# Kernel optimization log

Measured on AMD Instinct MI355X. Metric: run time of the kernel, lower is better.

Reference implementation:

```python
import jax, jax.numpy as jnp
import numpy as np

EPS = 1e-5
P, B, T, C = 2, 8, 1024, 1024
H = 4 * C

def layernorm(x, g, b):
    mu = jnp.mean(x, axis=-1, keepdims=True)
    var = jnp.var(x, axis=-1, keepdims=True)
    return (x - mu) * jax.lax.rsqrt(var + EPS) * g + b

def time_shift(x):
    # ZeroPad2d((0,0,1,-1)): xx[t] = x[t-1], xx[0] = 0 along the T axis
    pad = [(0, 0)] * (x.ndim - 2) + [(1, 0), (0, 0)]
    return jnp.pad(x, pad)[..., :-1, :]

def wkv(time_decay, time_first, k, v):
    # Faithful port of the RWKV-v4 CUDA WKV scan (numerically stable form).
    # k, v: [N, T, C]; time_decay/time_first: [C]
    w = -jnp.exp(time_decay)  # decay (negative)
    u = time_first
    kT = jnp.moveaxis(k, 1, 0)  # [T, N, C]
    vT = jnp.moveaxis(v, 1, 0)
    N = k.shape[0]
    Cc = k.shape[2]

    def step(carry, kv):
        aa, bb, pp = carry
        kk, vv = kv
        ww = u + kk
        p = jnp.maximum(pp, ww)
        e1 = jnp.exp(pp - p)
        e2 = jnp.exp(ww - p)
        y = (e1 * aa + e2 * vv) / (e1 * bb + e2)
        ww2 = w + pp
        p2 = jnp.maximum(ww2, kk)
        e1b = jnp.exp(ww2 - p2)
        e2b = jnp.exp(kk - p2)
        return (e1b * aa + e2b * vv, e1b * bb + e2b, p2), y

    init = (jnp.zeros((N, Cc), jnp.float32), jnp.zeros((N, Cc), jnp.float32),
            jnp.full((N, Cc), -1e38, jnp.float32))
    _, yT = jax.lax.scan(step, init, (kT, vT))
    return jnp.moveaxis(yT, 0, 1)  # [N, T, C]


def setup_inputs() -> dict:
    key = jax.random.key(0)
    ks = jax.random.split(key, 20)
    f32 = jnp.float32
    layer_id, n_layer = 1, 12
    ratio_0_to_1 = layer_id / (n_layer - 1)
    ratio_1_to_almost0 = 1.0 - layer_id / n_layer
    xcurve = (np.arange(C, dtype=np.float32) / C).reshape(1, 1, C)
    decay_speed = -5 + 8 * (np.arange(C, dtype=np.float32) / (C - 1)) ** (0.7 + 1.3 * ratio_0_to_1)
    zigzag = (np.array([(i + 1) % 3 - 1 for i in range(C)], dtype=np.float32)) * 0.5
    time_first = np.ones(C, dtype=np.float32) * np.log(0.3) + zigzag
    mk = np.stack([xcurve ** ratio_1_to_almost0 for _ in range(P)], 0)  # [P,1,1,C]
    mv = np.stack([xcurve ** ratio_1_to_almost0 + 0.3 * ratio_0_to_1 for _ in range(P)], 0)
    mr = np.stack([xcurve ** (0.5 * ratio_1_to_almost0) for _ in range(P)], 0)
    s = 0.02
    return {
        'x': jax.random.normal(ks[0], (P, B, T, C), f32),
        'ln1_g': jnp.ones((C,), f32), 'ln1_b': jnp.zeros((C,), f32),
        'ln2_g': jnp.ones((C,), f32), 'ln2_b': jnp.zeros((C,), f32),
        'time_decay': jnp.asarray(decay_speed, f32),
        'time_first': jnp.asarray(time_first, f32),
        'att_mix_k': jnp.asarray(mk, f32), 'att_mix_v': jnp.asarray(mv, f32),
        'att_mix_r': jnp.asarray(mr, f32),
        'Wk': jax.random.normal(ks[1], (C, C), f32) * s,
        'Wv': jax.random.normal(ks[2], (C, C), f32) * s,
        'Wr': jax.random.normal(ks[3], (C, C), f32) * s,
        'Wo': jax.random.normal(ks[4], (C, C), f32) * s,
        'cm_mix_k': jnp.asarray(mk, f32), 'cm_mix_r': jnp.asarray(mk, f32),
        'Wck': jax.random.normal(ks[5], (H, C), f32) * s,
        'Wcr': jax.random.normal(ks[6], (C, C), f32) * s,
        'Wcv': jax.random.normal(ks[7], (C, H), f32) * s,
    }


def reference(x, ln1_g, ln1_b, ln2_g, ln2_b, time_decay, time_first,
              att_mix_k, att_mix_v, att_mix_r, Wk, Wv, Wr, Wo,
              cm_mix_k, cm_mix_r, Wck, Wcr, Wcv):
    p, b, t, c = x.shape
    # --- TimeMix branch: x = x + Wo @ (sigmoid(r) * WKV(k, v)) ---
    h = layernorm(x, ln1_g, ln1_b)
    xx = time_shift(h)
    xk = h * att_mix_k + xx * (1 - att_mix_k)
    xv = h * att_mix_v + xx * (1 - att_mix_v)
    xr = h * att_mix_r + xx * (1 - att_mix_r)
    k = jnp.einsum('pbtc,dc->pbtd', xk, Wk)
    v = jnp.einsum('pbtc,dc->pbtd', xv, Wv)
    sr = jax.nn.sigmoid(jnp.einsum('pbtc,dc->pbtd', xr, Wr))
    y = wkv(time_decay, time_first,
            k.reshape(p * b, t, c), v.reshape(p * b, t, c)).reshape(p, b, t, c)
    x = x + jnp.einsum('pbtc,dc->pbtd', sr * y, Wo)
    # --- ChannelMix branch ---
    h = layernorm(x, ln2_g, ln2_b)
    xx = time_shift(h)
    xk = h * cm_mix_k + xx * (1 - cm_mix_k)
    xr = h * cm_mix_r + xx * (1 - cm_mix_r)
    kk = jnp.einsum('pbtc,hc->pbth', xk, Wck)
    kk = jnp.square(jax.nn.relu(kk))
    kv = jnp.einsum('pbth,ch->pbtc', kk, Wcv)
    out = jax.nn.sigmoid(jnp.einsum('pbtc,dc->pbtd', xr, Wcr)) * kv
    return x + out
```

## Files before the change

kernel.cpp:

```cpp
#include <hip/hip_runtime.h>

#define T_SEQ 1024
#define C_DIM 1024
#define H_DIM 4096
#define M_ROWS 16384
#define CHUNKS 16
#define CLEN 64

typedef _Float16 f16x8 __attribute__((ext_vector_type(8)));
typedef _Float16 f16x4 __attribute__((ext_vector_type(4)));
typedef float    f32x4 __attribute__((ext_vector_type(4)));

#define AS1 __attribute__((address_space(1)))
#define AS3 __attribute__((address_space(3)))

__device__ __forceinline__ void gload_lds16(const void* g, void* l) {
  __builtin_amdgcn_global_load_lds((const AS1 void*)g, (AS3 void*)l, 16, 0, 0);
}

__device__ __forceinline__ float sigmoidf_(float x) {
  return 1.0f / (1.0f + __expf(-x));
}

__global__ __launch_bounds__(256) void cvt_kernel(const float* __restrict__ in,
                                                  _Float16* __restrict__ out, int n4) {
  int i = blockIdx.x * 256 + threadIdx.x;
  if (i >= n4) return;
  f32x4 v = reinterpret_cast<const f32x4*>(in)[i];
  f16x4 o;
  o[0] = (_Float16)v[0]; o[1] = (_Float16)v[1];
  o[2] = (_Float16)v[2]; o[3] = (_Float16)v[3];
  reinterpret_cast<f16x4*>(out)[i] = o;
}

__global__ __launch_bounds__(256) void ln_kernel(const float* __restrict__ x,
    const float* __restrict__ g, const float* __restrict__ b,
    _Float16* __restrict__ h) {
  const int row  = blockIdx.x * 4 + (threadIdx.x >> 6);
  const int lane = threadIdx.x & 63;
  const f32x4* xr = reinterpret_cast<const f32x4*>(x + (size_t)row * C_DIM);
  f32x4 v[4];
  float s = 0.f, sq = 0.f;
#pragma unroll
  for (int i = 0; i < 4; ++i) {
    v[i] = xr[i * 64 + lane];
#pragma unroll
    for (int j = 0; j < 4; ++j) { s += v[i][j]; sq += v[i][j] * v[i][j]; }
  }
#pragma unroll
  for (int off = 32; off > 0; off >>= 1) {
    s  += __shfl_xor(s, off, 64);
    sq += __shfl_xor(sq, off, 64);
  }
  const float mu   = s * (1.0f / C_DIM);
  const float var  = sq * (1.0f / C_DIM) - mu * mu;
  const float rstd = rsqrtf(var + 1e-5f);
  const f32x4* g4 = reinterpret_cast<const f32x4*>(g);
  const f32x4* b4 = reinterpret_cast<const f32x4*>(b);
  f16x4* h4 = reinterpret_cast<f16x4*>(h + (size_t)row * C_DIM);
#pragma unroll
  for (int i = 0; i < 4; ++i) {
    f32x4 gg = g4[i * 64 + lane];
    f32x4 bb = b4[i * 64 + lane];
    f16x4 o;
#pragma unroll
    for (int j = 0; j < 4; ++j)
      o[j] = (_Float16)((v[i][j] - mu) * rstd * gg[j] + bb[j]);
    h4[i * 64 + lane] = o;
  }
}

__global__ __launch_bounds__(256) void mix3_kernel(const _Float16* __restrict__ h,
    const float* __restrict__ mk, const float* __restrict__ mv, const float* __restrict__ mr,
    _Float16* __restrict__ xk, _Float16* __restrict__ xv, _Float16* __restrict__ xr) {
  const int i  = blockIdx.x * 256 + threadIdx.x;
  const int m  = i >> 7;
  const int c0 = (i & 127) << 3;
  const int p  = m >> 13;
  const int t  = m & (T_SEQ - 1);
  const f16x8* h8 = reinterpret_cast<const f16x8*>(h);
  f16x8 hc = h8[i];
  f16x8 hp;
#pragma unroll
  for (int j = 0; j < 8; ++j) hp[j] = (_Float16)0.f;
  if (t) hp = h8[i - 128];
  f16x8 ok, ov, orr;
#pragma unroll
  for (int j = 0; j < 8; ++j) {
    const float hcf = (float)hc[j], hpf = (float)hp[j];
    const float a = mk[p * C_DIM + c0 + j];
    const float c = mv[p * C_DIM + c0 + j];
    const float d = mr[p * C_DIM + c0 + j];
    ok[j]  = (_Float16)(hcf * a + hpf * (1.f - a));
    ov[j]  = (_Float16)(hcf * c + hpf * (1.f - c));
    orr[j] = (_Float16)(hcf * d + hpf * (1.f - d));
  }
  reinterpret_cast<f16x8*>(xk)[i] = ok;
  reinterpret_cast<f16x8*>(xv)[i] = ov;
  reinterpret_cast<f16x8*>(xr)[i] = orr;
}

__global__ __launch_bounds__(256) void mix2_kernel(const _Float16* __restrict__ h,
    const float* __restrict__ mk, const float* __restrict__ mr,
    _Float16* __restrict__ xk, _Float16* __restrict__ xr) {
  const int i  = blockIdx.x * 256 + threadIdx.x;
  const int m  = i >> 7;
  const int c0 = (i & 127) << 3;
  const int p  = m >> 13;
  const int t  = m & (T_SEQ - 1);
  const f16x8* h8 = reinterpret_cast<const f16x8*>(h);
  f16x8 hc = h8[i];
  f16x8 hp;
#pragma unroll
  for (int j = 0; j < 8; ++j) hp[j] = (_Float16)0.f;
  if (t) hp = h8[i - 128];
  f16x8 ok, orr;
#pragma unroll
  for (int j = 0; j < 8; ++j) {
    const float hcf = (float)hc[j], hpf = (float)hp[j];
    const float a = mk[p * C_DIM + c0 + j];
    const float d = mr[p * C_DIM + c0 + j];
    ok[j]  = (_Float16)(hcf * a + hpf * (1.f - a));
    orr[j] = (_Float16)(hcf * d + hpf * (1.f - d));
  }
  reinterpret_cast<f16x8*>(xk)[i] = ok;
  reinterpret_cast<f16x8*>(xr)[i] = orr;
}

__global__ __launch_bounds__(1024, 1) void wkv_kernel(const _Float16* __restrict__ k,
    const _Float16* __restrict__ v, const _Float16* __restrict__ r,
    const float* __restrict__ td, const float* __restrict__ tf,
    _Float16* __restrict__ a_out) {
  __shared__ float sA[CHUNKS][64];
  __shared__ float sB[CHUNKS][64];
  __shared__ float sP[CHUNKS][64];
  const int tid   = threadIdx.x;
  const int chunk = tid >> 6;
  const int ch    = tid & 63;
  const int n     = blockIdx.x >> 4;
  const int cg    = blockIdx.x & 15;
  const int c     = cg * 64 + ch;
  const float w = -__expf(td[c]);
  const float u = tf[c];
  const size_t cbase = (size_t)n * T_SEQ * C_DIM + (size_t)chunk * CLEN * C_DIM + c;

  float aa = 0.f, bb = 0.f, pp = -1e38f;
  for (int s = 0; s < CLEN; ++s) {
    const size_t idx = cbase + (size_t)s * C_DIM;
    const float kk = (float)k[idx];
    const float vv = (float)v[idx];
    const float ww2 = w + pp;
    const float p2  = fmaxf(ww2, kk);
    const float e1b = __expf(ww2 - p2);
    const float e2b = __expf(kk - p2);
    aa = e1b * aa + e2b * vv;
    bb = e1b * bb + e2b;
    pp = p2;
  }
  sA[chunk][ch] = aa; sB[chunk][ch] = bb; sP[chunk][ch] = pp;
  __syncthreads();

  if (chunk == 0) {
    float pa = 0.f, pb = 0.f, ppr = -1e38f;
    const float wL = w * (float)CLEN;
    for (int j = 0; j < CHUNKS; ++j) {
      const float la = sA[j][ch], lb = sB[j][ch], lp = sP[j][ch];
      sA[j][ch] = pa; sB[j][ch] = pb; sP[j][ch] = ppr;
      const float dp = wL + ppr;
      const float np = fmaxf(dp, lp);
      const float e1 = __expf(dp - np);
      const float e2 = __expf(lp - np);
      pa  = e1 * pa + e2 * la;
      pb  = e1 * pb + e2 * lb;
      ppr = np;
    }
  }
  __syncthreads();

  aa = sA[chunk][ch]; bb = sB[chunk][ch]; pp = sP[chunk][ch];
  for (int s = 0; s < CLEN; ++s) {
    const size_t idx = cbase + (size_t)s * C_DIM;
    const float kk = (float)k[idx];
    const float vv = (float)v[idx];
    const float ww = u + kk;
    const float p  = fmaxf(pp, ww);
    const float e1 = __expf(pp - p);
    const float e2 = __expf(ww - p);
    const float yv = __fdividef(e1 * aa + e2 * vv, e1 * bb + e2);
    const float sr = sigmoidf_((float)r[idx]);
    a_out[idx] = (_Float16)(sr * yv);
    const float ww2 = w + pp;
    const float p2  = fmaxf(ww2, kk);
    const float e1b = __expf(ww2 - p2);
    const float e2b = __expf(kk - p2);
    aa = e1b * aa + e2b * vv;
    bb = e1b * bb + e2b;
    pp = p2;
  }
}

#define GBAR() do { __builtin_amdgcn_sched_barrier(0); \
                    __builtin_amdgcn_s_barrier(); \
                    __builtin_amdgcn_sched_barrier(0); } while (0)
#define WVN(n) do { asm volatile("s_waitcnt vmcnt(" #n ")" ::: "memory"); \
                    __builtin_amdgcn_sched_barrier(0); } while (0)
#define WL0()  do { asm volatile("s_waitcnt lgkmcnt(0)" ::: "memory"); \
                    __builtin_amdgcn_sched_barrier(0); } while (0)
#define STAGE(op, SRC, row0, k0, bb) do { \
    _Pragma("unroll") \
    for (int c_ = 0; c_ < 2; ++c_) { \
      gload_lds16((SRC) + (size_t)((row0) + c_ * 64) * K + (k0), \
                  &lds[bb][op][((size_t)((row0) + c_ * 64) << 6) + dbase]); \
    } } while (0)
#define RD_A(mh) do { \
    _Pragma("unroll") for (int i_ = 0; i_ < 4; ++i_) \
    _Pragma("unroll") for (int k_ = 0; k_ < 2; ++k_) \
      af[i_][k_] = *reinterpret_cast<const f16x8*>( \
        &lds[b][0][((wr * 128 + (mh) * 64 + i_ * 16 + frow) << 6) + \
                   (((k_ << 5) + fk) ^ fxorh)]); \
  } while (0)
#define RD_B(nh) do { \
    _Pragma("unroll") for (int j_ = 0; j_ < 2; ++j_) \
    _Pragma("unroll") for (int k_ = 0; k_ < 2; ++k_) \
      bf[j_][k_] = *reinterpret_cast<const f16x8*>( \
        &lds[b][1][((wcn * 64 + (nh) * 32 + j_ * 16 + frow) << 6) + \
                   (((k_ << 5) + fk) ^ fxorh)]); \
  } while (0)
#define MM(mh, nh) do { \
    __builtin_amdgcn_s_setprio(1); \
    _Pragma("unroll") for (int k_ = 0; k_ < 2; ++k_) \
    _Pragma("unroll") for (int i_ = 0; i_ < 4; ++i_) \
    _Pragma("unroll") for (int j_ = 0; j_ < 2; ++j_) \
      acc[(mh) * 4 + i_][(nh) * 2 + j_] = __builtin_amdgcn_mfma_f32_16x16x32_f16( \
        af[i_][k_], bf[j_][k_], acc[(mh) * 4 + i_][(nh) * 2 + j_], 0, 0, 0); \
    __builtin_amdgcn_s_setprio(0); \
  } while (0)

template<int EPI>
__global__ __launch_bounds__(512, 2) void gemm_nt_256(
    const _Float16* __restrict__ A, const _Float16* __restrict__ B,
    void* __restrict__ Cv, const float* __restrict__ X,
    const _Float16* __restrict__ KV, int M, int N, int K) {
  __shared__ _Float16 lds[2][2][256 * 64];
  const int tid  = threadIdx.x;
  const int wave = tid >> 6;
  const int lane = tid & 63;
  const int wr   = wave >> 2;
  const int wcn  = wave & 3;

  const unsigned nwx  = gridDim.x;
  const unsigned pery = gridDim.y >> 3;
  const unsigned id   = blockIdx.y * nwx + blockIdx.x;
  const unsigned xcd  = id & 7;
  const unsigned loc  = id >> 3;
  const size_t m0 = (size_t)(xcd * pery + loc / nwx) * 256;
  const size_t n0 = (size_t)(loc % nwx) * 256;

  const int srow  = tid >> 3;
  const int scolh = ((tid & 7) ^ (srow & 7)) << 3;
  const size_t dbase = (size_t)(srow & ~7) << 6;
  const _Float16* sA = A + (m0 + srow) * (size_t)K + scolh;
  const _Float16* sB = B + (n0 + srow) * (size_t)K + scolh;

  const int frow  = lane & 15;
  const int fk    = (lane >> 4) << 3;
  const int fxorh = (frow & 7) << 3;

  f32x4 acc[8][4];
#pragma unroll
  for (int i = 0; i < 8; ++i)
#pragma unroll
    for (int j = 0; j < 4; ++j) acc[i][j] = (f32x4){0.f, 0.f, 0.f, 0.f};

  STAGE(0, sA, 0, 0, 0); STAGE(0, sA, 128, 0, 0);
  STAGE(1, sB, 0, 0, 0); STAGE(1, sB, 128, 0, 0);

  const int NT = K >> 6;
  for (int t = 0; t < NT; ++t) {
    const int b  = t & 1;
    const int nb = b ^ 1;
    const int k1 = (t + 1) << 6;
    if (t + 1 < NT) {
      STAGE(0, sA, 0, k1, nb); STAGE(0, sA, 128, k1, nb);
      STAGE(1, sB, 0, k1, nb); STAGE(1, sB, 128, k1, nb);
      WVN(8);
    } else {
      WVN(0);
    }
    GBAR();
    f16x8 af[4][2], bf[2][2];
    RD_A(0); RD_B(0); WL0(); MM(0, 0);
    RD_B(1);          WL0(); MM(0, 1);
    RD_A(1); RD_B(0); WL0(); MM(1, 0);
    RD_B(1);          WL0(); MM(1, 1);
    GBAR();
  }

  const int ecol  = lane & 15;
  const int erow4 = (lane >> 4) * 4;
#pragma unroll
  for (int mf = 0; mf < 8; ++mf)
#pragma unroll
    for (int nf = 0; nf < 4; ++nf) {
      const size_t rbase = m0 + (size_t)(wr * 128 + mf * 16 + erow4);
      const size_t cc    = n0 + (size_t)(wcn * 64 + nf * 16 + ecol);
#pragma unroll
      for (int r = 0; r < 4; ++r) {
        const float val = acc[mf][nf][r];
        const size_t off = (rbase + r) * (size_t)N + cc;
        if constexpr (EPI == 0) {
          ((_Float16*)Cv)[off] = (_Float16)val;
        } else if constexpr (EPI == 1) {
          const float tq = fmaxf(val, 0.f);
          ((_Float16*)Cv)[off] = (_Float16)(tq * tq);
        } else if constexpr (EPI == 2) {
          ((float*)Cv)[off] = val + X[off];
        } else {
          ((float*)Cv)[off] = X[off] + sigmoidf_(val) * (float)KV[off];
        }
      }
    }
}

extern "C" void kernel_launch(void* const* d_in, const int* in_sizes, int n_in,
                              void* d_out, int out_size, void* d_ws, size_t ws_size,
                              hipStream_t stream) {
  const float* x      = (const float*)d_in[0];
  const float* ln1_g  = (const float*)d_in[1];
  const float* ln1_b  = (const float*)d_in[2];
  const float* ln2_g  = (const float*)d_in[3];
  const float* ln2_b  = (const float*)d_in[4];
  const float* tdec   = (const float*)d_in[5];
  const float* tfirst = (const float*)d_in[6];
  const float* amk    = (const float*)d_in[7];
  const float* amv    = (const float*)d_in[8];
  const float* amr    = (const float*)d_in[9];
  const float* Wk     = (const float*)d_in[10];
  const float* Wv     = (const float*)d_in[11];
  const float* Wr     = (const float*)d_in[12];
  const float* Wo     = (const float*)d_in[13];
  const float* cmk    = (const float*)d_in[14];
  const float* cmr    = (const float*)d_in[15];
  const float* Wck    = (const float*)d_in[16];
  const float* Wcr    = (const float*)d_in[17];
  const float* Wcv    = (const float*)d_in[18];

  char* ws = (char*)d_ws;
  const size_t SZ = (size_t)M_ROWS * C_DIM * sizeof(_Float16);
  _Float16* B0 = (_Float16*)(ws + 0 * SZ);
  _Float16* B1 = (_Float16*)(ws + 1 * SZ);
  _Float16* B2 = (_Float16*)(ws + 2 * SZ);
  _Float16* B3 = (_Float16*)(ws + 3 * SZ);
  _Float16* B4 = (_Float16*)(ws + 4 * SZ);
  _Float16* B5 = (_Float16*)(ws + 5 * SZ);
  _Float16* B6 = (_Float16*)(ws + 6 * SZ);
  _Float16* wWk  = (_Float16*)(ws + 7 * SZ);
  _Float16* wWv  = wWk  + (size_t)C_DIM * C_DIM;
  _Float16* wWr  = wWv  + (size_t)C_DIM * C_DIM;
  _Float16* wWo  = wWr  + (size_t)C_DIM * C_DIM;
  _Float16* wWcr = wWo  + (size_t)C_DIM * C_DIM;
  _Float16* wWck = wWcr + (size_t)C_DIM * C_DIM;
  _Float16* wWcv = wWck + (size_t)H_DIM * C_DIM;

  auto cvt = [&](const float* src, _Float16* dst, size_t n) {
    const int n4 = (int)(n / 4);
    cvt_kernel<<<dim3((n4 + 255) / 256), dim3(256), 0, stream>>>(src, dst, n4);
  };
  cvt(Wk,  wWk,  (size_t)C_DIM * C_DIM);
  cvt(Wv,  wWv,  (size_t)C_DIM * C_DIM);
  cvt(Wr,  wWr,  (size_t)C_DIM * C_DIM);
  cvt(Wo,  wWo,  (size_t)C_DIM * C_DIM);
  cvt(Wcr, wWcr, (size_t)C_DIM * C_DIM);
  cvt(Wck, wWck, (size_t)H_DIM * C_DIM);
  cvt(Wcv, wWcv, (size_t)C_DIM * H_DIM);

  const dim3 blk(256);
  const dim3 gblk(512);
  const dim3 gN1(C_DIM / 256, M_ROWS / 256);
  const dim3 gN4(H_DIM / 256, M_ROWS / 256);

  ln_kernel<<<dim3(M_ROWS / 4), blk, 0, stream>>>(x, ln1_g, ln1_b, B0);
  mix3_kernel<<<dim3(M_ROWS * 128 / 256), blk, 0, stream>>>(B0, amk, amv, amr, B1, B2, B3);
  gemm_nt_256<0><<<gN1, gblk, 0, stream>>>(B1, wWk, B4, nullptr, nullptr, M_ROWS, C_DIM, C_DIM);
  gemm_nt_256<0><<<gN1, gblk, 0, stream>>>(B2, wWv, B5, nullptr, nullptr, M_ROWS, C_DIM, C_DIM);
  gemm_nt_256<0><<<gN1, gblk, 0, stream>>>(B3, wWr, B6, nullptr, nullptr, M_ROWS, C_DIM, C_DIM);
  wkv_kernel<<<dim3(256), dim3(1024), 0, stream>>>(B4, B5, B6, tdec, tfirst, B1);
  gemm_nt_256<2><<<gN1, gblk, 0, stream>>>(B1, wWo, d_out, x, nullptr, M_ROWS, C_DIM, C_DIM);

  ln_kernel<<<dim3(M_ROWS / 4), blk, 0, stream>>>((const float*)d_out, ln2_g, ln2_b, B0);
  mix2_kernel<<<dim3(M_ROWS * 128 / 256), blk, 0, stream>>>(B0, cmk, cmr, B1, B2);
  gemm_nt_256<1><<<gN4, gblk, 0, stream>>>(B1, wWck, B3, nullptr, nullptr, M_ROWS, H_DIM, C_DIM);
  gemm_nt_256<0><<<gN1, gblk, 0, stream>>>(B3, wWcv, B1, nullptr, nullptr, M_ROWS, C_DIM, H_DIM);
  gemm_nt_256<3><<<gN1, gblk, 0, stream>>>(B2, wWcr, d_out, (const float*)d_out, B1,
                                           M_ROWS, C_DIM, C_DIM);
}
```

Baseline: 680.6 us.

## Batch weight conversions into one launch and restructure GEMM LDS read schedule

The seven fp32-to-fp16 weight conversion launches are merged into a single kernel that picks its source and destination segment from the block index, removing per-launch overhead. In the GEMM inner loop, all B fragments and both A halves are now read from LDS up front into separate registers. A partial lgkmcnt wait lets the first half's MFMAs start while the second half's reads are still in flight. This replaces four full LDS waits per k-tile with two, at the cost of more live fragment registers, which may pressure the 2-waves-per-SIMD occupancy target.

```diff
diff --git a/kernel.cpp b/kernel.cpp
--- a/kernel.cpp
+++ b/kernel.cpp
@@ -22,15 +22,25 @@
   return 1.0f / (1.0f + __expf(-x));
 }
 
-__global__ __launch_bounds__(256) void cvt_kernel(const float* __restrict__ in,
-                                                  _Float16* __restrict__ out, int n4) {
-  int i = blockIdx.x * 256 + threadIdx.x;
-  if (i >= n4) return;
-  f32x4 v = reinterpret_cast<const f32x4*>(in)[i];
+struct CvtArgs {
+  const float* src[7];
+  _Float16*    dst[7];
+  int n4[7];
+  int start[8];
+};
+
+__global__ __launch_bounds__(256) void cvt_all_kernel(CvtArgs a) {
+  const int bid = blockIdx.x;
+  int s = 0;
+#pragma unroll
+  for (int j = 0; j < 7; ++j) s += (bid >= a.start[j + 1]) ? 1 : 0;
+  const int i = (bid - a.start[s]) * 256 + threadIdx.x;
+  if (i >= a.n4[s]) return;
+  f32x4 v = reinterpret_cast<const f32x4*>(a.src[s])[i];
   f16x4 o;
   o[0] = (_Float16)v[0]; o[1] = (_Float16)v[1];
   o[2] = (_Float16)v[2]; o[3] = (_Float16)v[3];
-  reinterpret_cast<f16x4*>(out)[i] = o;
+  reinterpret_cast<f16x4*>(a.dst[s])[i] = o;
 }
 
 __global__ __launch_bounds__(256) void ln_kernel(const float* __restrict__ x,
@@ -204,35 +214,36 @@
                     __builtin_amdgcn_sched_barrier(0); } while (0)
 #define WVN(n) do { asm volatile("s_waitcnt vmcnt(" #n ")" ::: "memory"); \
                     __builtin_amdgcn_sched_barrier(0); } while (0)
-#define WL0()  do { asm volatile("s_waitcnt lgkmcnt(0)" ::: "memory"); \
+#define WLN(n) do { asm volatile("s_waitcnt lgkmcnt(" #n ")" ::: "memory"); \
                     __builtin_amdgcn_sched_barrier(0); } while (0)
+#define SCHED() __builtin_amdgcn_sched_barrier(0)
 #define STAGE(op, SRC, row0, k0, bb) do { \
     _Pragma("unroll") \
     for (int c_ = 0; c_ < 2; ++c_) { \
       gload_lds16((SRC) + (size_t)((row0) + c_ * 64) * K + (k0), \
                   &lds[bb][op][((size_t)((row0) + c_ * 64) << 6) + dbase]); \
     } } while (0)
-#define RD_A(mh) do { \
+#define RD_AH(dst, mh) do { \
     _Pragma("unroll") for (int i_ = 0; i_ < 4; ++i_) \
     _Pragma("unroll") for (int k_ = 0; k_ < 2; ++k_) \
-      af[i_][k_] = *reinterpret_cast<const f16x8*>( \
+      dst[i_][k_] = *reinterpret_cast<const f16x8*>( \
         &lds[b][0][((wr * 128 + (mh) * 64 + i_ * 16 + frow) << 6) + \
                    (((k_ << 5) + fk) ^ fxorh)]); \
   } while (0)
-#define RD_B(nh) do { \
-    _Pragma("unroll") for (int j_ = 0; j_ < 2; ++j_) \
+#define RD_BALL() do { \
+    _Pragma("unroll") for (int j_ = 0; j_ < 4; ++j_) \
     _Pragma("unroll") for (int k_ = 0; k_ < 2; ++k_) \
       bf[j_][k_] = *reinterpret_cast<const f16x8*>( \
-        &lds[b][1][((wcn * 64 + (nh) * 32 + j_ * 16 + frow) << 6) + \
+        &lds[b][1][((wcn * 64 + j_ * 16 + frow) << 6) + \
                    (((k_ << 5) + fk) ^ fxorh)]); \
   } while (0)
-#define MM(mh, nh) do { \
+#define MM32(src, mh) do { \
     __builtin_amdgcn_s_setprio(1); \
     _Pragma("unroll") for (int k_ = 0; k_ < 2; ++k_) \
     _Pragma("unroll") for (int i_ = 0; i_ < 4; ++i_) \
-    _Pragma("unroll") for (int j_ = 0; j_ < 2; ++j_) \
-      acc[(mh) * 4 + i_][(nh) * 2 + j_] = __builtin_amdgcn_mfma_f32_16x16x32_f16( \
-        af[i_][k_], bf[j_][k_], acc[(mh) * 4 + i_][(nh) * 2 + j_], 0, 0, 0); \
+    _Pragma("unroll") for (int j_ = 0; j_ < 4; ++j_) \
+      acc[(mh) * 4 + i_][j_] = __builtin_amdgcn_mfma_f32_16x16x32_f16( \
+        src[i_][k_], bf[j_][k_], acc[(mh) * 4 + i_][j_], 0, 0, 0); \
     __builtin_amdgcn_s_setprio(0); \
   } while (0)
 
@@ -288,11 +299,14 @@
       WVN(0);
     }
     GBAR();
-    f16x8 af[4][2], bf[2][2];
-    RD_A(0); RD_B(0); WL0(); MM(0, 0);
-    RD_B(1);          WL0(); MM(0, 1);
-    RD_A(1); RD_B(0); WL0(); MM(1, 0);
-    RD_B(1);          WL0(); MM(1, 1);
+    f16x8 a0[4][2], a1[4][2], bf[4][2];
+    RD_AH(a0, 0); RD_BALL();
+    SCHED();
+    RD_AH(a1, 1);
+    WLN(8);
+    MM32(a0, 0);
+    WLN(0);
+    MM32(a1, 1);
     GBAR();
   }
 
@@ -362,17 +376,24 @@
   _Float16* wWck = wWcr + (size_t)C_DIM * C_DIM;
   _Float16* wWcv = wWck + (size_t)H_DIM * C_DIM;
 
-  auto cvt = [&](const float* src, _Float16* dst, size_t n) {
-    const int n4 = (int)(n / 4);
-    cvt_kernel<<<dim3((n4 + 255) / 256), dim3(256), 0, stream>>>(src, dst, n4);
-  };
-  cvt(Wk,  wWk,  (size_t)C_DIM * C_DIM);
-  cvt(Wv,  wWv,  (size_t)C_DIM * C_DIM);
-  cvt(Wr,  wWr,  (size_t)C_DIM * C_DIM);
-  cvt(Wo,  wWo,  (size_t)C_DIM * C_DIM);
-  cvt(Wcr, wWcr, (size_t)C_DIM * C_DIM);
-  cvt(Wck, wWck, (size_t)H_DIM * C_DIM);
-  cvt(Wcv, wWcv, (size_t)C_DIM * H_DIM);
+  {
+    CvtArgs a;
+    const float* srcs[7] = {Wk, Wv, Wr, Wo, Wcr, Wck, Wcv};
+    _Float16*    dsts[7] = {wWk, wWv, wWr, wWo, wWcr, wWck, wWcv};
+    const size_t ns[7]   = {(size_t)C_DIM * C_DIM, (size_t)C_DIM * C_DIM,
+                            (size_t)C_DIM * C_DIM, (size_t)C_DIM * C_DIM,
+                            (size_t)C_DIM * C_DIM, (size_t)H_DIM * C_DIM,
+                            (size_t)C_DIM * H_DIM};
+    int st = 0;
+    for (int j = 0; j < 7; ++j) {
+      a.src[j] = srcs[j]; a.dst[j] = dsts[j];
+      a.n4[j] = (int)(ns[j] / 4);
+      a.start[j] = st;
+      st += (a.n4[j] + 255) / 256;
+    }
+    a.start[7] = st;
+    cvt_all_kernel<<<dim3(st), dim3(256), 0, stream>>>(a);
+  }
 
   const dim3 blk(256);
   const dim3 gblk(512);
```

New measurement: 668.6 us. About the same (-1.8%).
